# Kernel tuning notes

Measured on AMD Instinct MI355X. Metric: run time of the kernel, lower is better.

## Reference

```python
import jax, jax.numpy as jnp
import numpy as np
from jax import lax

A = 3          # anchors per scale
C = 80         # num foreground classes (COCO)
NMS_THRESH = 0.45
NMS_TOPK = 400
POST_NMS = 100


def setup_inputs() -> dict:
    key = jax.random.key(0)
    k0, k1, k2 = jax.random.split(key, 3)
    B = 8
    ch = A * (C + 5)  # 255
    # raw head outputs (pre-decode conv activations), modest scale so exp() stays sane
    tip0 = jax.random.normal(k0, (B, ch, 19, 19), jnp.float32) * 0.5
    tip1 = jax.random.normal(k1, (B, ch, 38, 38), jnp.float32) * 0.5
    tip2 = jax.random.normal(k2, (B, ch, 76, 76), jnp.float32) * 0.5
    # standard YOLOv3 COCO anchors, deepest scale (stride 32) first
    anchors0 = jnp.array([[116., 90.], [156., 198.], [373., 326.]], jnp.float32)
    anchors1 = jnp.array([[30., 61.], [62., 45.], [59., 119.]], jnp.float32)
    anchors2 = jnp.array([[10., 13.], [16., 30.], [33., 23.]], jnp.float32)
    return dict(tip0=tip0, tip1=tip1, tip2=tip2,
                anchors0=anchors0, anchors1=anchors1, anchors2=anchors2)


def _decode(tip, anchors, stride):
    """YOLOOutputV3 inference decode. tip: (B, A*(C+5), H, W)."""
    B, _, H, W = tip.shape
    # (B, A*(C+5), H*W) -> (B, H*W, A, C+5)
    pred = tip.reshape(B, A * (C + 5), H * W).transpose(0, 2, 1).reshape(B, H * W, A, C + 5)
    gx, gy = jnp.meshgrid(jnp.arange(W), jnp.arange(H))       # each (H, W)
    offsets = jnp.stack([gx, gy], -1).reshape(1, H * W, 1, 2).astype(tip.dtype)
    centers = (jax.nn.sigmoid(pred[..., :2]) + offsets) * stride          # (B,HW,A,2)
    scales = jnp.exp(pred[..., 2:4]) * anchors.reshape(1, 1, A, 2)        # (B,HW,A,2)
    conf = jax.nn.sigmoid(pred[..., 4:5])                                 # objectness
    cls_scores = jax.nn.sigmoid(pred[..., 5:]) * conf                      # (B,HW,A,C)
    wh = scales * 0.5
    bbox = jnp.concatenate([centers - wh, centers + wh], -1)               # corner format
    return bbox.reshape(B, H * W * A, 4), cls_scores.reshape(B, H * W * A, C)


def _pairwise_iou(b):
    """b: (K,4) corner boxes -> (K,K) IoU."""
    x1, y1, x2, y2 = b[:, 0], b[:, 1], b[:, 2], b[:, 3]
    area = jnp.maximum(x2 - x1, 0.) * jnp.maximum(y2 - y1, 0.)
    iw = jnp.maximum(jnp.minimum(x2[:, None], x2[None, :]) - jnp.maximum(x1[:, None], x1[None, :]), 0.)
    ih = jnp.maximum(jnp.minimum(y2[:, None], y2[None, :]) - jnp.maximum(y1[:, None], y1[None, :]), 0.)
    inter = iw * ih
    return inter / (area[:, None] + area[None, :] - inter + 1e-12)


def _nms_single(det):
    """Class-aware greedy NMS on one image. det: (M,6) = (cid, score, x1,y1,x2,y2)."""
    K = NMS_TOPK
    _, idx = lax.top_k(det[:, 1], K)     # sort by score, keep top K
    d = det[idx]                          # (K,6), descending score
    iou = _pairwise_iou(d[:, 2:6])
    same = d[:, 0][:, None] == d[:, 0][None, :]   # only same class suppresses
    valid = d[:, 1] > 0.
    rng = jnp.arange(K)

    def body(i, keep):
        sup = (iou[i] > NMS_THRESH) & same[i] & (rng > i) & keep[i] & valid[i]
        return keep & ~sup

    keep = lax.fori_loop(0, K, body, jnp.ones((K,), bool)) & valid
    d = jnp.where(keep[:, None], d, jnp.full_like(d, -1.))
    order = jnp.argsort(-d[:, 1])         # kept (sorted) first, suppressed (-1) last
    return d[order][:POST_NMS]            # (POST_NMS, 6)


def _detect(tip0, tip1, tip2, anchors0, anchors1, anchors2):
    dets = []
    for tip, anc, stride in ((tip0, anchors0, 32), (tip1, anchors1, 16), (tip2, anchors2, 8)):
        bbox, scores = _decode(tip, anc, stride)          # (B,N,4), (B,N,C)
        B, N, _ = bbox.shape
        ids = jnp.broadcast_to(jnp.arange(C, dtype=bbox.dtype)[None, None, :, None], (B, N, C, 1))
        sc = scores[..., None]                            # (B,N,C,1)
        bx = jnp.broadcast_to(bbox[:, :, None, :], (B, N, C, 4))
        dets.append(jnp.concatenate([ids, sc, bx], -1).reshape(B, N * C, 6))
    det = jnp.concatenate(dets, 1)                        # (B, M, 6)
    return jax.vmap(_nms_single)(det)                     # (B, POST_NMS, 6)


def reference(tip0, tip1, tip2, anchors0, anchors1, anchors2):
    res = _detect(tip0, tip1, tip2, anchors0, anchors1, anchors2)
    ids = res[..., 0:1]
    scores = res[..., 1:2]
    bboxes = res[..., 2:6]
    return ids, scores, bboxes
```

## Files before the change

### kernel.cpp

```cpp
#include <hip/hip_runtime.h>
#include <stdint.h>

#define NUMA 3
#define NUMC 80
#define CAP  49152
#define CAP2 8192
#define KTOP 400
#define POST 100
#define NBIN1 2048
#define EQCAP 1024
#define KEY0 0x3EE66666u
#define LBUF 2048
#define NMASK (KTOP * 7)

typedef float f32x4 __attribute__((ext_vector_type(4)));

__device__ __forceinline__ float sigmoidf_(float x) { return 1.0f / (1.0f + expf(-x)); }
__device__ __forceinline__ unsigned uminu(unsigned a, unsigned b) { return a < b ? a : b; }

__global__ void init_kernel(unsigned* __restrict__ p) {
    int i = blockIdx.x * blockDim.x + threadIdx.x;
    if (i < NBIN1 * 16 + 40) p[i] = 0;
}

__global__ __launch_bounds__(256) void score_main(
        const float* __restrict__ t0, const float* __restrict__ t1,
        const float* __restrict__ t2,
        unsigned* __restrict__ ccnt, unsigned* __restrict__ ckey,
        unsigned* __restrict__ cidx, unsigned* __restrict__ histN)
{
    __shared__ unsigned lkey[LBUF], lidx[LBUF];
    __shared__ unsigned lh[NBIN1];
    __shared__ unsigned lcnt, lbase;
    const int tid = threadIdx.x;
    if (tid == 0) lcnt = 0;
    for (int i = tid; i < NBIN1; i += 256) lh[i] = 0;
    __syncthreads();

    const int ba = blockIdx.z;
    const int b = ba / 3, a = ba - 3 * b;
    const int c0 = blockIdx.y * 8;
    const int cx = blockIdx.x;

    #define LEMIT(SC, IDX) do { \
        unsigned key_ = __float_as_uint(SC); \
        if (key_ >= KEY0) { \
            atomicAdd(&lh[(key_ - KEY0) >> 13], 1u); \
            unsigned pos_ = atomicAdd(&lcnt, 1u); \
            if (pos_ < LBUF) { lkey[pos_] = key_; lidx[pos_] = (IDX); } \
        } \
    } while (0)

    if (cx < 2) {
        const int hw = cx * 256 + tid;
        if (hw < 361) {
            const float* base = t0 + (size_t)(b * 255 + a * 85) * 361;
            float cr = base[4 * 361 + hw];
            const float* p0 = base + (size_t)(5 + c0) * 361 + hw;
            float x0 = p0[0 * 361], x1 = p0[1 * 361], x2 = p0[2 * 361], x3 = p0[3 * 361];
            float x4 = p0[4 * 361], x5 = p0[5 * 361], x6 = p0[6 * 361], x7 = p0[7 * 361];
            float cf = sigmoidf_(cr);
            unsigned ib = (unsigned)((hw * NUMA + a) * NUMC + c0);
            LEMIT(sigmoidf_(x0) * cf, ib + 0);
            LEMIT(sigmoidf_(x1) * cf, ib + 1);
            LEMIT(sigmoidf_(x2) * cf, ib + 2);
            LEMIT(sigmoidf_(x3) * cf, ib + 3);
            LEMIT(sigmoidf_(x4) * cf, ib + 4);
            LEMIT(sigmoidf_(x5) * cf, ib + 5);
            LEMIT(sigmoidf_(x6) * cf, ib + 6);
            LEMIT(sigmoidf_(x7) * cf, ib + 7);
        }
    } else {
        const float* tip; int vHW, v, candOff;
        if (cx < 4) { tip = t1; vHW = 361;  v = (cx - 2) * 256 + tid; candOff = 86640; }
        else        { tip = t2; vHW = 1444; v = (cx - 4) * 256 + tid; candOff = 433200; }
        if (v < vHW) {
            const f32x4* bp = (const f32x4*)(tip + (size_t)(b * 255 + a * 85) * (size_t)(vHW * 4));
            f32x4 cv = bp[(size_t)4 * vHW + v];
            const f32x4* p0 = bp + (size_t)(5 + c0) * vHW + v;
            f32x4 s0 = p0[0 * (size_t)vHW], s1 = p0[1 * (size_t)vHW];
            f32x4 s2 = p0[2 * (size_t)vHW], s3 = p0[3 * (size_t)vHW];
            f32x4 s4 = p0[4 * (size_t)vHW], s5 = p0[5 * (size_t)vHW];
            f32x4 s6 = p0[6 * (size_t)vHW], s7 = p0[7 * (size_t)vHW];
            float cf0 = sigmoidf_(cv[0]), cf1 = sigmoidf_(cv[1]);
            float cf2 = sigmoidf_(cv[2]), cf3 = sigmoidf_(cv[3]);
            unsigned ib0 = (unsigned)(candOff + (v * 4 * NUMA + a) * NUMC + c0);
            #define EMIT4(S, U) do { \
                unsigned ib = ib0 + (U); \
                LEMIT(sigmoidf_((S)[0]) * cf0, ib); \
                LEMIT(sigmoidf_((S)[1]) * cf1, ib + 240); \
                LEMIT(sigmoidf_((S)[2]) * cf2, ib + 480); \
                LEMIT(sigmoidf_((S)[3]) * cf3, ib + 720); \
            } while (0)
            EMIT4(s0, 0); EMIT4(s1, 1); EMIT4(s2, 2); EMIT4(s3, 3);
            EMIT4(s4, 4); EMIT4(s5, 5); EMIT4(s6, 6); EMIT4(s7, 7);
            #undef EMIT4
        }
    }
    #undef LEMIT

    __syncthreads();
    if (tid == 0) {
        unsigned c = lcnt;
        if (c > LBUF) {
            atomicOr(&ccnt[b], 0x80000000u);
            lbase = 0xFFFFFFFFu;
        } else {
            lbase = atomicAdd(&ccnt[b], c);
        }
    }
    __syncthreads();
    unsigned c = uminu(lcnt, (unsigned)LBUF);
    unsigned basep = lbase;
    if (basep != 0xFFFFFFFFu) {
        for (unsigned i = tid; i < c; i += 256) {
            unsigned p = basep + i;
            if (p < CAP) {
                ckey[(size_t)b * CAP + p] = lkey[i];
                cidx[(size_t)b * CAP + p] = lidx[i];
            }
        }
    }
    unsigned* gh = histN + b * NBIN1;
    for (int i = tid; i < NBIN1; i += 256) {
        unsigned v2 = lh[i];
        if (v2) atomicAdd(&gh[i], v2);
    }
}

__device__ __forceinline__ void wave_select(const unsigned* h, int nbins, unsigned rank,
                                            unsigned* resv, int tid)
{
    if (tid >= 64) return;
    const int lane = tid;
    const int cs = nbins >> 6;
    unsigned v = 0;
    for (int k = 0; k < cs; k++) {
        int off = (k + lane) & (cs - 1);
        v += h[lane * cs + off];
    }
    unsigned S = v;
    #pragma unroll
    for (int o = 1; o < 64; o <<= 1) {
        unsigned t = (unsigned)__shfl_down((int)S, o);
        if (lane + o < 64) S += t;
    }
    unsigned long long bm = __ballot(S >= rank);
    if (bm == 0ull) bm = 1ull;
    int C = 63 - __builtin_clzll(bm);
    unsigned SC = (unsigned)__builtin_amdgcn_readlane((int)S, C);
    unsigned vC = (unsigned)__builtin_amdgcn_readlane((int)v, C);
    unsigned rem = rank - (SC - vC);
    unsigned w = (lane < cs) ? h[C * cs + lane] : 0u;
    unsigned T = w;
    #pragma unroll
    for (int o = 1; o < 64; o <<= 1) {
        unsigned t = (unsigned)__shfl_down((int)T, o);
        if (lane + o < 64) T += t;
    }
    unsigned long long bm2 = __ballot((T >= rem) && (lane < cs));
    if (bm2 == 0ull) bm2 = 1ull;
    int B = 63 - __builtin_clzll(bm2);
    unsigned TB = (unsigned)__builtin_amdgcn_readlane((int)T, B);
    unsigned wB = (unsigned)__builtin_amdgcn_readlane((int)w, B);
    if (lane == 0) {
        resv[0] = (unsigned)(C * cs + B);
        resv[1] = rem - (TB - wB);
    }
}

__global__ __launch_bounds__(256) void findcut_v(const unsigned* __restrict__ histN,
                                                 unsigned* __restrict__ cutfloor,
                                                 unsigned* __restrict__ ccnt,
                                                 unsigned* __restrict__ flags) {
    __shared__ unsigned h[NBIN1];
    __shared__ unsigned resv[2];
    int b = blockIdx.x;
    for (int i = threadIdx.x; i < NBIN1; i += 256) h[i] = histN[b * NBIN1 + i];
    __syncthreads();
    wave_select(h, NBIN1, KTOP, resv, threadIdx.x);
    __syncthreads();
    if (threadIdx.x == 0) {
        unsigned c = ccnt[b];
        bool ok = (c >= KTOP) && (c <= CAP);
        flags[b] = ok ? 1u : 0u;
        if (ok) {
            cutfloor[b] = KEY0 + (resv[0] << 13);
        } else {
            cutfloor[b] = 0u;
            ccnt[b] = 0;
        }
    }
}

__global__ __launch_bounds__(256) void fb_hist(
        const float* __restrict__ t0, const float* __restrict__ t1,
        const float* __restrict__ t2,
        unsigned* __restrict__ histF, const unsigned* __restrict__ flags)
{
    const int ba = blockIdx.z;
    const int b = ba / 3, a = ba - 3 * b;
    if (flags[b]) return;
    __shared__ unsigned lh[NBIN1];
    const int tid = threadIdx.x;
    for (int i = tid; i < NBIN1; i += 256) lh[i] = 0;
    __syncthreads();
    const int c0 = blockIdx.y * 8;
    const int cx = blockIdx.x;
    if (cx < 2) {
        const int hw = cx * 256 + tid;
        if (hw < 361) {
            const float* base = t0 + (size_t)(b * 255 + a * 85) * 361;
            float cf = sigmoidf_(base[4 * 361 + hw]);
            for (int u = 0; u < 8; u++) {
                float sc = sigmoidf_(base[(size_t)(5 + c0 + u) * 361 + hw]) * cf;
                atomicAdd(&lh[__float_as_uint(sc) >> 19], 1u);
            }
        }
    } else {
        const float* tip; int vHW, v;
        if (cx < 4) { tip = t1; vHW = 361;  v = (cx - 2) * 256 + tid; }
        else        { tip = t2; vHW = 1444; v = (cx - 4) * 256 + tid; }
        if (v < vHW) {
            const f32x4* bp = (const f32x4*)(tip + (size_t)(b * 255 + a * 85) * (size_t)(vHW * 4));
            f32x4 cv = bp[(size_t)4 * vHW + v];
            float cf[4] = { sigmoidf_(cv[0]), sigmoidf_(cv[1]), sigmoidf_(cv[2]), sigmoidf_(cv[3]) };
            for (int u = 0; u < 8; u++) {
                f32x4 s = bp[(size_t)(5 + c0 + u) * vHW + v];
                for (int l = 0; l < 4; l++)
                    atomicAdd(&lh[__float_as_uint(sigmoidf_(s[l]) * cf[l]) >> 19], 1u);
            }
        }
    }
    __syncthreads();
    unsigned* gh = histF + b * NBIN1;
    for (int i = tid; i < NBIN1; i += 256) {
        unsigned v2 = lh[i];
        if (v2) atomicAdd(&gh[i], v2);
    }
}

__global__ __launch_bounds__(256) void fb_cut(const unsigned* __restrict__ histF,
                                              unsigned* __restrict__ cutb,
                                              const unsigned* __restrict__ flags) {
    int b = blockIdx.x;
    if (flags[b]) return;
    __shared__ unsigned h[NBIN1];
    __shared__ unsigned resv[2];
    for (int i = threadIdx.x; i < NBIN1; i += 256) h[i] = histF[b * NBIN1 + i];
    __syncthreads();
    wave_select(h, NBIN1, KTOP, resv, threadIdx.x);
    __syncthreads();
    if (threadIdx.x == 0) cutb[b] = resv[0];
}

__global__ __launch_bounds__(256) void fb_compact(
        const float* __restrict__ t0, const float* __restrict__ t1,
        const float* __restrict__ t2,
        const unsigned* __restrict__ cutb, unsigned* __restrict__ ccnt,
        unsigned* __restrict__ ckey, unsigned* __restrict__ cidx,
        const unsigned* __restrict__ flags)
{
    const int ba = blockIdx.z;
    const int b = ba / 3, a = ba - 3 * b;
    if (flags[b]) return;
    const int tid = threadIdx.x;
    const int c0 = blockIdx.y * 8;
    const int cx = blockIdx.x;
    unsigned cutkey = cutb[b] << 19;

    if (cx < 2) {
        const int hw = cx * 256 + tid;
        if (hw < 361) {
            const float* base = t0 + (size_t)(b * 255 + a * 85) * 361;
            float cf = sigmoidf_(base[4 * 361 + hw]);
            for (int u = 0; u < 8; u++) {
                float sc = sigmoidf_(base[(size_t)(5 + c0 + u) * 361 + hw]) * cf;
                unsigned key = __float_as_uint(sc);
                if (key >= cutkey) {
                    unsigned pos = atomicAdd(&ccnt[b], 1u);
                    if (pos < CAP) {
                        ckey[(size_t)b * CAP + pos] = key;
                        cidx[(size_t)b * CAP + pos] = (unsigned)((hw * NUMA + a) * NUMC + c0 + u);
                    }
                }
            }
        }
    } else {
        const float* tip; int vHW, v, candOff;
        if (cx < 4) { tip = t1; vHW = 361;  v = (cx - 2) * 256 + tid; candOff = 86640; }
        else        { tip = t2; vHW = 1444; v = (cx - 4) * 256 + tid; candOff = 433200; }
        if (v < vHW) {
            const f32x4* bp = (const f32x4*)(tip + (size_t)(b * 255 + a * 85) * (size_t)(vHW * 4));
            f32x4 cv = bp[(size_t)4 * vHW + v];
            float cf[4] = { sigmoidf_(cv[0]), sigmoidf_(cv[1]), sigmoidf_(cv[2]), sigmoidf_(cv[3]) };
            unsigned ib0 = (unsigned)(candOff + (v * 4 * NUMA + a) * NUMC + c0);
            for (int u = 0; u < 8; u++) {
                f32x4 s = bp[(size_t)(5 + c0 + u) * vHW + v];
                for (int l = 0; l < 4; l++) {
                    float sc = sigmoidf_(s[l]) * cf[l];
                    unsigned key = __float_as_uint(sc);
                    if (key >= cutkey) {
                        unsigned pos = atomicAdd(&ccnt[b], 1u);
                        if (pos < CAP) {
                            ckey[(size_t)b * CAP + pos] = key;
                            cidx[(size_t)b * CAP + pos] = ib0 + (unsigned)u + (unsigned)l * 240;
                        }
                    }
                }
            }
        }
    }
}

__global__ __launch_bounds__(256) void prefilter(
        const unsigned* __restrict__ ckey, const unsigned* __restrict__ cidx,
        const unsigned* __restrict__ ccnt, const unsigned* __restrict__ cutfloor,
        unsigned* __restrict__ cnt2, unsigned* __restrict__ ckey2,
        unsigned* __restrict__ cidx2)
{
    __shared__ unsigned lk[LBUF], li[LBUF];
    __shared__ unsigned lcnt, lbase;
    const int tid = threadIdx.x;
    const int b = blockIdx.z;
    if (tid == 0) lcnt = 0;
    __syncthreads();
    const unsigned n = uminu(ccnt[b], (unsigned)CAP);
    const unsigned cutf = cutfloor[b];
    const unsigned* ck = ckey + (size_t)b * CAP;
    const unsigned* ci = cidx + (size_t)b * CAP;
    for (unsigned i = blockIdx.x * 256 + tid; i < n; i += 32 * 256) {
        unsigned k = ck[i];
        if (k >= cutf) {
            unsigned p = atomicAdd(&lcnt, 1u);
            if (p < LBUF) { lk[p] = k; li[p] = ci[i]; }
        }
    }
    __syncthreads();
    if (tid == 0) lbase = atomicAdd(&cnt2[b], uminu(lcnt, (unsigned)LBUF));
    __syncthreads();
    unsigned c = uminu(lcnt, (unsigned)LBUF);
    for (unsigned i = tid; i < c; i += 256) {
        unsigned p = lbase + i;
        if (p < CAP2) {
            ckey2[(size_t)b * CAP2 + p] = lk[i];
            cidx2[(size_t)b * CAP2 + p] = li[i];
        }
    }
}

__global__ __launch_bounds__(512) void topk_kernel(
        const float* __restrict__ t0, const float* __restrict__ t1,
        const float* __restrict__ t2,
        const float* __restrict__ anc0, const float* __restrict__ anc1,
        const float* __restrict__ anc2,
        const unsigned* __restrict__ ckey, const unsigned* __restrict__ cidx,
        const unsigned* __restrict__ ccnt,
        const unsigned* __restrict__ ckey2, const unsigned* __restrict__ cidx2,
        const unsigned* __restrict__ cnt2,
        float* __restrict__ dX1, float* __restrict__ dY1,
        float* __restrict__ dX2, float* __restrict__ dY2,
        float* __restrict__ dSC, unsigned* __restrict__ dCID)
{
    const int b = blockIdx.x;
    const int tid = threadIdx.x;
    const int T = 512;

    __shared__ unsigned hist[4096];
    __shared__ unsigned resv[2];
    __shared__ unsigned selk[512], seli[512];
    __shared__ unsigned eqi[EQCAP];
    __shared__ unsigned cnts[2];

    unsigned n2 = cnt2[b];
    const unsigned* ck; const unsigned* ci; unsigned n;
    if (n2 <= (unsigned)CAP2) {
        ck = ckey2 + (size_t)b * CAP2; ci = cidx2 + (size_t)b * CAP2; n = n2;
    } else {
        ck = ckey + (size_t)b * CAP; ci = cidx + (size_t)b * CAP;
        n = uminu(ccnt[b], (unsigned)CAP);
    }

    for (int i = tid; i < NBIN1; i += T) hist[i] = 0;
    __syncthreads();
    for (unsigned i = tid; i < n; i += T) atomicAdd(&hist[ck[i] >> 19], 1u);
    __syncthreads();
    wave_select(hist, NBIN1, KTOP, resv, tid);
    __syncthreads();
    unsigned b1 = resv[0], r2 = resv[1];
    __syncthreads();

    for (int i = tid; i < 4096; i += T) hist[i] = 0;
    __syncthreads();
    for (unsigned i = tid; i < n; i += T) {
        unsigned k = ck[i];
        if ((k >> 19) == b1) atomicAdd(&hist[(k >> 7) & 0xFFFu], 1u);
    }
    __syncthreads();
    wave_select(hist, 4096, r2, resv, tid);
    __syncthreads();
    unsigned b2 = resv[0], r3 = resv[1];
    __syncthreads();

    for (int i = tid; i < 128; i += T) hist[i] = 0;
    __syncthreads();
    unsigned pref = (b1 << 12) | b2;
    for (unsigned i = tid; i < n; i += T) {
        unsigned k = ck[i];
        if ((k >> 7) == pref) atomicAdd(&hist[k & 127u], 1u);
    }
    __syncthreads();
    wave_select(hist, 128, r3, resv, tid);
    __syncthreads();
    unsigned b3 = resv[0], needEq = resv[1];
    unsigned K400 = (b1 << 19) | (b2 << 7) | b3;
    __syncthreads();

    selk[tid] = 0u; seli[tid] = 0xFFFFFFFFu;
    for (int i = tid; i < EQCAP; i += T) eqi[i] = 0xFFFFFFFFu;
    if (tid == 0) { cnts[0] = 0; cnts[1] = 0; }
    __syncthreads();
    for (unsigned i = tid; i < n; i += T) {
        unsigned k = ck[i];
        if (k > K400) {
            unsigned p = atomicAdd(&cnts[0], 1u);
            if (p < KTOP) { selk[p] = k; seli[p] = ci[i]; }
        } else if (k == K400) {
            unsigned q = atomicAdd(&cnts[1], 1u);
            if (q < EQCAP) eqi[q] = ci[i];
        }
    }
    __syncthreads();
    unsigned selCnt = uminu(cnts[0], (unsigned)KTOP);
    unsigned eqN   = uminu(cnts[1], (unsigned)EQCAP);

    if (eqN > needEq) {
        int P2 = 1; while ((unsigned)P2 < eqN) P2 <<= 1;
        for (int k2 = 2; k2 <= P2; k2 <<= 1) {
            for (int j = k2 >> 1; j > 0; j >>= 1) {
                __syncthreads();
                for (int i = tid; i < P2; i += T) {
                    int ixj = i ^ j;
                    if (ixj > i && ixj < P2) {
                        unsigned va = eqi[i], vb = eqi[ixj];
                        bool up = ((i & k2) == 0);
                        if (up ? (va > vb) : (va < vb)) { eqi[i] = vb; eqi[ixj] = va; }
                    }
                }
            }
        }
        __syncthreads();
    }
    for (unsigned t2v = tid; t2v < needEq; t2v += T) {
        unsigned p = selCnt + t2v;
        if (p < KTOP) { selk[p] = K400; seli[p] = eqi[t2v]; }
    }
    __syncthreads();

    for (int k2 = 2; k2 <= 512; k2 <<= 1) {
        int j = k2 >> 1;
        for (; j >= 64; j >>= 1) {
            __syncthreads();
            int i = tid, ixj = i ^ j;
            if (ixj > i) {
                unsigned ka = selk[i], kb = selk[ixj], ia = seli[i], ib = seli[ixj];
                bool before = (ka > kb) || (ka == kb && ia < ib);
                bool up = ((i & k2) == 0);
                if (up ? !before : before) {
                    selk[i] = kb; selk[ixj] = ka; seli[i] = ib; seli[ixj] = ia;
                }
            }
        }
        __syncthreads();
        for (; j > 0; j >>= 1) {
            int i = tid, ixj = i ^ j;
            if (ixj > i) {
                unsigned ka = selk[i], kb = selk[ixj], ia = seli[i], ib = seli[ixj];
                bool before = (ka > kb) || (ka == kb && ia < ib);
                bool up = ((i & k2) == 0);
                if (up ? !before : before) {
                    selk[i] = kb; selk[ixj] = ka; seli[i] = ib; seli[ixj] = ia;
                }
            }
        }
    }
    __syncthreads();

    if (tid < KTOP) {
        unsigned idx = seli[tid];
        const float* tip; const float* anc; int HW, W, candOff; float strideF;
        if (idx < 86640u)       { tip = t0; anc = anc0; HW = 361;  W = 19; strideF = 32.f; candOff = 0; }
        else if (idx < 433200u) { tip = t1; anc = anc1; HW = 1444; W = 38; strideF = 16.f; candOff = 86640; }
        else                    { tip = t2; anc = anc2; HW = 5776; W = 76; strideF = 8.f;  candOff = 433200; }
        unsigned local = idx - (unsigned)candOff;
        int cls = (int)(local % NUMC);
        int nn  = (int)(local / NUMC);
        int a = nn % NUMA, hwl = nn / NUMA;
        const float* base = tip + (size_t)(b * 255 + a * 85) * HW + hwl;
        float tx = base[0];
        float ty = base[(size_t)HW];
        float tw = base[(size_t)2 * HW];
        float th = base[(size_t)3 * HW];
        float fx = (float)(hwl % W), fy = (float)(hwl / W);
        float cx = (sigmoidf_(tx) + fx) * strideF;
        float cy = (sigmoidf_(ty) + fy) * strideF;
        float hw_ = expf(tw) * anc[2 * a]     * 0.5f;
        float hh_ = expf(th) * anc[2 * a + 1] * 0.5f;
        int o = b * KTOP + tid;
        dX1[o] = cx - hw_; dY1[o] = cy - hh_;
        dX2[o] = cx + hw_; dY2[o] = cy + hh_;
        dSC[o] = __uint_as_float(selk[tid]);
        dCID[o] = (unsigned)cls;
    }
}

__global__ __launch_bounds__(256) void mask_kernel(
        const float* __restrict__ dX1, const float* __restrict__ dY1,
        const float* __restrict__ dX2, const float* __restrict__ dY2,
        const unsigned* __restrict__ dCID, unsigned long long* __restrict__ maskG)
{
    __shared__ float lx1[KTOP], ly1[KTOP], lx2[KTOP], ly2[KTOP];
    __shared__ int lcid[KTOP];
    const int b = blockIdx.y;
    const int tid = threadIdx.x;
    for (int i = tid; i < KTOP; i += 256) {
        int o = b * KTOP + i;
        lx1[i] = dX1[o]; ly1[i] = dY1[o];
        lx2[i] = dX2[o]; ly2[i] = dY2[o];
        lcid[i] = (int)dCID[o];
    }
    __syncthreads();
    int p = blockIdx.x * 256 + tid;
    if (p < NMASK) {
        int i = p / 7, w = p - i * 7;
        float x1i = lx1[i], y1i = ly1[i], x2i = lx2[i], y2i = ly2[i];
        float ai = fmaxf(x2i - x1i, 0.f) * fmaxf(y2i - y1i, 0.f);
        int cidI = lcid[i];
        unsigned long long m = 0ull;
        int j0 = w * 64;
        int j1 = j0 + 64; if (j1 > KTOP) j1 = KTOP;
        int js = j0 > i + 1 ? j0 : i + 1;
        for (int j = js; j < j1; j++) {
            if (lcid[j] != cidI) continue;
            float iw = fminf(x2i, lx2[j]) - fmaxf(x1i, lx1[j]);
            float ih = fminf(y2i, ly2[j]) - fmaxf(y1i, ly1[j]);
            iw = fmaxf(iw, 0.f); ih = fmaxf(ih, 0.f);
            float inter = iw * ih;
            float aj = fmaxf(lx2[j] - lx1[j], 0.f) * fmaxf(ly2[j] - ly1[j], 0.f);
            float iou = inter / (ai + aj - inter + 1e-12f);
            if (iou > 0.45f) m |= (1ull << (j - j0));
        }
        maskG[(size_t)b * NMASK + p] = m;
    }
}

__global__ __launch_bounds__(512) void greedy_kernel(
        const float* __restrict__ dX1, const float* __restrict__ dY1,
        const float* __restrict__ dX2, const float* __restrict__ dY2,
        const float* __restrict__ dSC, const unsigned* __restrict__ dCID,
        const unsigned long long* __restrict__ maskG, float* __restrict__ out)
{
    __shared__ unsigned long long maskL[NMASK];
    __shared__ unsigned long long vkeep[7];
    __shared__ float oid[POST], osc[POST], obb[POST * 4];
    const int b = blockIdx.x;
    const int tid = threadIdx.x;

    for (int i = tid; i < NMASK; i += 512) maskL[i] = maskG[(size_t)b * NMASK + i];
    if (tid < POST) { oid[tid] = -1.f; osc[tid] = -1.f; }
    if (tid < POST * 4) obb[tid] = -1.f;
    __syncthreads();

    if (tid < 64) {
        const int lane = tid;
        unsigned long long keep = 0ull;
        if (lane < 7) keep = (lane == 6) ? 0xFFFFull : ~0ull;
        unsigned long long mb[8];
        #pragma unroll
        for (int k = 0; k < 8; k++)
            mb[k] = (lane < 7) ? maskL[k * 7 + lane] : 0ull;
        for (int ib = 0; ib < KTOP; ib += 8) {
            #pragma unroll
            for (int k = 0; k < 8; k++) {
                int i = ib + k;
                unsigned long long m = mb[k];
                int nf = ib + 8 + k;
                mb[k] = (lane < 7 && nf < KTOP) ? maskL[nf * 7 + lane] : 0ull;
                int w = i >> 6;
                unsigned klo = (unsigned)__builtin_amdgcn_readlane((int)(unsigned)(keep & 0xFFFFFFFFull), w);
                unsigned khi = (unsigned)__builtin_amdgcn_readlane((int)(unsigned)(keep >> 32), w);
                unsigned long long kw = ((unsigned long long)khi << 32) | klo;
                if ((kw >> (i & 63)) & 1ull) keep &= ~m;
            }
        }
        if (lane < 7) vkeep[lane] = keep;
    }
    __syncthreads();

    if (tid < KTOP) {
        int w = tid >> 6, bp = tid & 63;
        unsigned long long kw = vkeep[w];
        if ((kw >> bp) & 1ull) {
            int r = 0;
            for (int q = 0; q < w; q++) r += __popcll(vkeep[q]);
            r += __popcll(kw & ((1ull << bp) - 1ull));
            if (r < POST) {
                int o = b * KTOP + tid;
                oid[r] = (float)(int)dCID[o];
                osc[r] = dSC[o];
                obb[r * 4 + 0] = dX1[o];
                obb[r * 4 + 1] = dY1[o];
                obb[r * 4 + 2] = dX2[o];
                obb[r * 4 + 3] = dY2[o];
            }
        }
    }
    __syncthreads();
    if (tid < POST) {
        out[b * POST + tid]       = oid[tid];
        out[800 + b * POST + tid] = osc[tid];
    }
    if (tid < POST * 4) out[1600 + b * POST * 4 + tid] = obb[tid];
}

extern "C" void kernel_launch(void* const* d_in, const int* in_sizes, int n_in,
                              void* d_out, int out_size, void* d_ws, size_t ws_size,
                              hipStream_t stream)
{
    const float* tip0 = (const float*)d_in[0];
    const float* tip1 = (const float*)d_in[1];
    const float* tip2 = (const float*)d_in[2];
    const float* anc0 = (const float*)d_in[3];
    const float* anc1 = (const float*)d_in[4];
    const float* anc2 = (const float*)d_in[5];
    float* out = (float*)d_out;

    unsigned* histN    = (unsigned*)d_ws;
    unsigned* histF    = histN + 8 * NBIN1;
    unsigned* cutb     = histF + 8 * NBIN1;
    unsigned* cutfloor = cutb + 8;
    unsigned* ccnt     = cutfloor + 8;
    unsigned* cnt2     = ccnt + 8;
    unsigned* flags    = cnt2 + 8;
    unsigned* ckey     = flags + 8;
    unsigned* cidx     = ckey + (size_t)8 * CAP;
    unsigned* ckey2    = cidx + (size_t)8 * CAP;
    unsigned* cidx2    = ckey2 + (size_t)8 * CAP2;
    float*    dX1      = (float*)(cidx2 + (size_t)8 * CAP2);
    float*    dY1      = dX1 + 8 * KTOP;
    float*    dX2      = dY1 + 8 * KTOP;
    float*    dY2      = dX2 + 8 * KTOP;
    float*    dSC      = dY2 + 8 * KTOP;
    unsigned* dCID     = (unsigned*)(dSC + 8 * KTOP);
    unsigned long long* maskG = (unsigned long long*)(dCID + 8 * KTOP);

    init_kernel<<<(NBIN1 * 16 + 40 + 255) / 256, 256, 0, stream>>>(histN);

    dim3 g(10, 10, 24);
    score_main<<<g, 256, 0, stream>>>(tip0, tip1, tip2, ccnt, ckey, cidx, histN);
    findcut_v<<<8, 256, 0, stream>>>(histN, cutfloor, ccnt, flags);
    fb_hist<<<g, 256, 0, stream>>>(tip0, tip1, tip2, histF, flags);
    fb_cut<<<8, 256, 0, stream>>>(histF, cutb, flags);
    fb_compact<<<g, 256, 0, stream>>>(tip0, tip1, tip2, cutb, ccnt, ckey, cidx, flags);
    prefilter<<<dim3(32, 1, 8), 256, 0, stream>>>(ckey, cidx, ccnt, cutfloor,
                                                  cnt2, ckey2, cidx2);
    topk_kernel<<<8, 512, 0, stream>>>(tip0, tip1, tip2, anc0, anc1, anc2,
                                       ckey, cidx, ccnt, ckey2, cidx2, cnt2,
                                       dX1, dY1, dX2, dY2, dSC, dCID);
    mask_kernel<<<dim3((NMASK + 255) / 256, 8), 256, 0, stream>>>(
        dX1, dY1, dX2, dY2, dCID, maskG);
    greedy_kernel<<<8, 512, 0, stream>>>(dX1, dY1, dX2, dY2, dSC, dCID, maskG, out);
}
```

Baseline: 196.8 us.

## Build score histogram in findcut from compacted keys instead of score_main

Removes the per-block shared-memory histogram and the global histogram atomics from score_main, and halves its LDS staging buffer so more blocks fit per CU. findcut_v now reads the compacted candidate keys per batch with 1024 threads and builds the histogram itself. This moves histogram work from the wide scoring pass into a small 8-block kernel, which may become serial if candidate counts are large. The smaller LBUF also raises the chance of local buffer overflow, which would drop candidates.

```diff
diff --git a/kernel.cpp b/kernel.cpp
--- a/kernel.cpp
+++ b/kernel.cpp
@@ -10,7 +10,7 @@
 #define NBIN1 2048
 #define EQCAP 1024
 #define KEY0 0x3EE66666u
-#define LBUF 2048
+#define LBUF 1024
 #define NMASK (KTOP * 7)
 
 typedef float f32x4 __attribute__((ext_vector_type(4)));
@@ -27,14 +27,12 @@
         const float* __restrict__ t0, const float* __restrict__ t1,
         const float* __restrict__ t2,
         unsigned* __restrict__ ccnt, unsigned* __restrict__ ckey,
-        unsigned* __restrict__ cidx, unsigned* __restrict__ histN)
+        unsigned* __restrict__ cidx)
 {
     __shared__ unsigned lkey[LBUF], lidx[LBUF];
-    __shared__ unsigned lh[NBIN1];
     __shared__ unsigned lcnt, lbase;
     const int tid = threadIdx.x;
     if (tid == 0) lcnt = 0;
-    for (int i = tid; i < NBIN1; i += 256) lh[i] = 0;
     __syncthreads();
 
     const int ba = blockIdx.z;
@@ -45,7 +43,6 @@
     #define LEMIT(SC, IDX) do { \
         unsigned key_ = __float_as_uint(SC); \
         if (key_ >= KEY0) { \
-            atomicAdd(&lh[(key_ - KEY0) >> 13], 1u); \
             unsigned pos_ = atomicAdd(&lcnt, 1u); \
             if (pos_ < LBUF) { lkey[pos_] = key_; lidx[pos_] = (IDX); } \
         } \
@@ -121,11 +118,6 @@
             }
         }
     }
-    unsigned* gh = histN + b * NBIN1;
-    for (int i = tid; i < NBIN1; i += 256) {
-        unsigned v2 = lh[i];
-        if (v2) atomicAdd(&gh[i], v2);
-    }
 }
 
 __device__ __forceinline__ void wave_select(const unsigned* h, int nbins, unsigned rank,
@@ -169,20 +161,29 @@
     }
 }
 
-__global__ __launch_bounds__(256) void findcut_v(const unsigned* __restrict__ histN,
-                                                 unsigned* __restrict__ cutfloor,
-                                                 unsigned* __restrict__ ccnt,
-                                                 unsigned* __restrict__ flags) {
+__global__ __launch_bounds__(1024) void findcut_v(const unsigned* __restrict__ ckey,
+                                                  unsigned* __restrict__ cutfloor,
+                                                  unsigned* __restrict__ ccnt,
+                                                  unsigned* __restrict__ flags) {
     __shared__ unsigned h[NBIN1];
     __shared__ unsigned resv[2];
     int b = blockIdx.x;
-    for (int i = threadIdx.x; i < NBIN1; i += 256) h[i] = histN[b * NBIN1 + i];
-    __syncthreads();
-    wave_select(h, NBIN1, KTOP, resv, threadIdx.x);
-    __syncthreads();
-    if (threadIdx.x == 0) {
-        unsigned c = ccnt[b];
-        bool ok = (c >= KTOP) && (c <= CAP);
+    int tid = threadIdx.x;
+    for (int i = tid; i < NBIN1; i += 1024) h[i] = 0;
+    unsigned c = ccnt[b];
+    bool ok = (c >= KTOP) && (c <= CAP);
+    __syncthreads();
+    if (ok) {
+        const unsigned* ck = ckey + (size_t)b * CAP;
+        for (unsigned i = tid; i < c; i += 1024) {
+            unsigned bin = (ck[i] - KEY0) >> 13;
+            atomicAdd(&h[uminu(bin, NBIN1 - 1)], 1u);
+        }
+    }
+    __syncthreads();
+    wave_select(h, NBIN1, KTOP, resv, tid);
+    __syncthreads();
+    if (tid == 0) {
         flags[b] = ok ? 1u : 0u;
         if (ok) {
             cutfloor[b] = KEY0 + (resv[0] << 13);
@@ -319,7 +320,7 @@
         unsigned* __restrict__ cnt2, unsigned* __restrict__ ckey2,
         unsigned* __restrict__ cidx2)
 {
-    __shared__ unsigned lk[LBUF], li[LBUF];
+    __shared__ unsigned lk[2048], li[2048];
     __shared__ unsigned lcnt, lbase;
     const int tid = threadIdx.x;
     const int b = blockIdx.z;
@@ -333,13 +334,13 @@
         unsigned k = ck[i];
         if (k >= cutf) {
             unsigned p = atomicAdd(&lcnt, 1u);
-            if (p < LBUF) { lk[p] = k; li[p] = ci[i]; }
-        }
-    }
-    __syncthreads();
-    if (tid == 0) lbase = atomicAdd(&cnt2[b], uminu(lcnt, (unsigned)LBUF));
-    __syncthreads();
-    unsigned c = uminu(lcnt, (unsigned)LBUF);
+            if (p < 2048u) { lk[p] = k; li[p] = ci[i]; }
+        }
+    }
+    __syncthreads();
+    if (tid == 0) lbase = atomicAdd(&cnt2[b], uminu(lcnt, 2048u));
+    __syncthreads();
+    unsigned c = uminu(lcnt, 2048u);
     for (unsigned i = tid; i < c; i += 256) {
         unsigned p = lbase + i;
         if (p < CAP2) {
@@ -657,8 +658,8 @@
     init_kernel<<<(NBIN1 * 16 + 40 + 255) / 256, 256, 0, stream>>>(histN);
 
     dim3 g(10, 10, 24);
-    score_main<<<g, 256, 0, stream>>>(tip0, tip1, tip2, ccnt, ckey, cidx, histN);
-    findcut_v<<<8, 256, 0, stream>>>(histN, cutfloor, ccnt, flags);
+    score_main<<<g, 256, 0, stream>>>(tip0, tip1, tip2, ccnt, ckey, cidx);
+    findcut_v<<<8, 1024, 0, stream>>>(ckey, cutfloor, ccnt, flags);
     fb_hist<<<g, 256, 0, stream>>>(tip0, tip1, tip2, histF, flags);
     fb_cut<<<8, 256, 0, stream>>>(histF, cutb, flags);
     fb_compact<<<g, 256, 0, stream>>>(tip0, tip1, tip2, cutb, ccnt, ckey, cidx, flags);
```

New measurement: 204.1 us. 1.04x slower.
